# Kernel optimization log

Measured on AMD Instinct MI355X. Metric: run time of the kernel, lower is better.

The kernel has to match this reference:

```python
import jax, jax.numpy as jnp
import numpy as np

EPS = 1e-5
N_HEADS = 8


def _ln(x, g, b):
    m = jnp.mean(x, -1, keepdims=True)
    v = jnp.mean((x - m) ** 2, -1, keepdims=True)
    return (x - m) * jax.lax.rsqrt(v + EPS) * g + b


def setup_inputs() -> dict:
    key = jax.random.key(0)
    ks = jax.random.split(key, 24)
    B, T, H = 64, 512, 256
    HH, H2 = H // 2, 2 * H
    w = lambda k, shape, fan_in: jax.random.normal(k, shape, jnp.float32) / np.sqrt(fan_in)
    return {
        "state": jax.random.normal(ks[0], (B, T, H), jnp.float32),
        "action": jax.random.normal(ks[1], (B, T, 2), jnp.float32),
        "ae_w1": w(ks[2], (2, HH), 2), "ae_b1": jnp.zeros((HH,), jnp.float32),
        "ae_w2": w(ks[3], (HH, H), HH), "ae_b2": jnp.zeros((H,), jnp.float32),
        "ln1_g": jnp.ones((H,), jnp.float32), "ln1_b": jnp.zeros((H,), jnp.float32),
        "ln2_g": jnp.ones((H,), jnp.float32), "ln2_b": jnp.zeros((H,), jnp.float32),
        "wq": w(ks[4], (H, H), H), "bq": jnp.zeros((H,), jnp.float32),
        "wk": w(ks[5], (H, H), H), "bk": jnp.zeros((H,), jnp.float32),
        "wv": w(ks[6], (H, H), H), "bv": jnp.zeros((H,), jnp.float32),
        "wo": w(ks[7], (H, H), H), "bo": jnp.zeros((H,), jnp.float32),
        "gru_wih": w(ks[8], (H, 3 * H2), H), "gru_bih": jnp.zeros((3 * H2,), jnp.float32),
        "gru_whh": w(ks[9], (H2, 3 * H2), H2), "gru_bhh": jnp.zeros((3 * H2,), jnp.float32),
        "mlp_w": w(ks[10], (H2, H), H2), "mlp_b": jnp.zeros((H,), jnp.float32),
    }


def reference(state, action, ae_w1, ae_b1, ae_w2, ae_b2, ln1_g, ln1_b, ln2_g, ln2_b,
              wq, bq, wk, bk, wv, bv, wo, bo,
              gru_wih, gru_bih, gru_whh, gru_bhh, mlp_w, mlp_b):
    B, T, H = state.shape
    dH = H // N_HEADS
    # action encoder (vectorized over all timesteps at once)
    ae = jax.nn.relu(action @ ae_w1 + ae_b1) @ ae_w2 + ae_b2  # [B,T,H]
    q_in = _ln(state, ln1_g, ln1_b)
    kv_in = _ln(ae, ln2_g, ln2_b)
    qh = (q_in @ wq + bq).reshape(B, T, N_HEADS, dH)
    kh = (kv_in @ wk + bk).reshape(B, T, N_HEADS, dH)
    vh = (kv_in @ wv + bv).reshape(B, T, N_HEADS, dH)
    # single query / single key per (b,t): softmax over the length-1 key axis == 1
    scores = jnp.sum(qh * kh, -1, keepdims=True) / jnp.sqrt(jnp.asarray(dH, state.dtype))
    attn = jax.nn.softmax(scores, axis=-1)  # [B,T,nH,1] of ones
    attended = (attn * vh).reshape(B, T, H) @ wo + bo
    x = state + attended  # [B,T,H]
    # GRU: original uses batch_first=False on a [B,T,H] tensor, so the
    # recurrence runs over dim 0 (B) with T as the effective batch.
    H2 = gru_whh.shape[0]

    def step(h, x_t):  # h,[T,2H]; x_t [T,H]
        gi = x_t @ gru_wih + gru_bih
        gh = h @ gru_whh + gru_bhh
        i_r, i_z, i_n = jnp.split(gi, 3, -1)
        h_r, h_z, h_n = jnp.split(gh, 3, -1)
        r = jax.nn.sigmoid(i_r + h_r)
        z = jax.nn.sigmoid(i_z + h_z)
        n = jnp.tanh(i_n + r * h_n)
        h_new = (1.0 - z) * n + z * h
        return h_new, h_new

    h0 = jnp.zeros((T, H2), x.dtype)
    _, out = jax.lax.scan(step, h0, x)  # [B,T,2H]
    states = out @ mlp_w + mlp_b  # dropout is identity in eval mode
    return states, states[:, -1]
```

## Files before the change

kernel.cpp:

```cpp
#include <hip/hip_runtime.h>
#include <hip/hip_bf16.h>

typedef unsigned short u16;
typedef unsigned long long u64;
typedef __attribute__((ext_vector_type(8))) short bf16x8;
typedef __attribute__((ext_vector_type(4))) float f32x4;

static __device__ __forceinline__ u16 f2bf(float f) {
    union { float f; unsigned u; } cv; cv.f = f;
    unsigned u = cv.u;
    unsigned r = u + 0x7FFF + ((u >> 16) & 1);
    return (u16)(r >> 16);
}
static __device__ __forceinline__ float bf2f(u16 b) {
    union { unsigned u; float f; } cv; cv.u = ((unsigned)b) << 16;
    return cv.f;
}
static __device__ __forceinline__ float sigmoidf_(float x) {
    return 1.0f / (1.0f + __expf(-x));
}

__global__ __launch_bounds__(256) void transpose_tile_bf(
    const float* __restrict__ src, u16* __restrict__ dst, int K, int N)
{
    __shared__ u16 t[64][66];
    int k0 = blockIdx.x * 64, n0 = blockIdx.y * 64;
    int tid = threadIdx.x;
    int r = tid >> 4, c4 = (tid & 15) * 4;
#pragma unroll
    for (int p = 0; p < 4; ++p) {
        int row = r + p * 16;
        float4 v = *(const float4*)&src[(size_t)(k0 + row) * N + n0 + c4];
        t[c4 + 0][row] = f2bf(v.x);
        t[c4 + 1][row] = f2bf(v.y);
        t[c4 + 2][row] = f2bf(v.z);
        t[c4 + 3][row] = f2bf(v.w);
    }
    __syncthreads();
    int rr = tid >> 3, cc = (tid & 7) * 8;
#pragma unroll
    for (int p = 0; p < 2; ++p) {
        int row = rr + p * 32;
        u16 pack[8];
#pragma unroll
        for (int j = 0; j < 8; ++j) pack[j] = t[row][cc + j];
        *(uint4*)&dst[(size_t)(n0 + row) * K + k0 + cc] = *(uint4*)pack;
    }
}

__global__ __launch_bounds__(256) void convert_bf(
    const float* __restrict__ src, u16* __restrict__ dst)
{
    int i = (blockIdx.x * 256 + threadIdx.x) * 4;
    float4 v = *(const float4*)&src[i];
    u16 pack[4] = { f2bf(v.x), f2bf(v.y), f2bf(v.z), f2bf(v.w) };
    *(u64*)&dst[i] = *(u64*)pack;
}

__global__ __launch_bounds__(256) void bias_fuse(
    const float* __restrict__ bv, const float* __restrict__ wo,
    const float* __restrict__ bo, float* __restrict__ bfv)
{
    int j = threadIdx.x;
    float t = bo[j];
    for (int k = 0; k < 256; ++k) t = fmaf(bv[k], wo[k * 256 + j], t);
    bfv[j] = t;
}

__global__ __launch_bounds__(256) void ae_ln_mfma(
    const float* __restrict__ action,
    const float* __restrict__ w1, const float* __restrict__ b1,
    const u16* __restrict__ w2T, const float* __restrict__ b2,
    const float* __restrict__ g, const float* __restrict__ be,
    u16* __restrict__ kvbf)
{
    __shared__ u16 lB[256][136];
    __shared__ u16 lA[64][136];
    int tid = threadIdx.x;
    long base = (long)blockIdx.x * 64;

    for (int idx = tid; idx < 256 * 16; idx += 256) {
        int r = idx >> 4, ch = (idx & 15) * 8;
        *(uint4*)&lB[r][ch] = *(const uint4*)&w2T[r * 128 + ch];
    }
    for (int idx = tid; idx < 8192; idx += 256) {
        int r = idx >> 7, k = idx & 127;
        float a0 = action[(base + r) * 2], a1 = action[(base + r) * 2 + 1];
        float v = fmaf(a1, w1[128 + k], fmaf(a0, w1[k], b1[k]));
        lA[r][k] = f2bf(v > 0.f ? v : 0.f);
    }
    __syncthreads();

    int wv = tid >> 6, l = tid & 63;
    int fr = l & 15, fq = l >> 4;
    f32x4 acc[4][4] = {};
#pragma unroll
    for (int ks = 0; ks < 4; ++ks) {
        bf16x8 a[4], b[4];
#pragma unroll
        for (int mi = 0; mi < 4; ++mi) a[mi] = *(bf16x8*)&lA[mi * 16 + fr][ks * 32 + fq * 8];
#pragma unroll
        for (int ni = 0; ni < 4; ++ni) b[ni] = *(bf16x8*)&lB[wv * 64 + ni * 16 + fr][ks * 32 + fq * 8];
#pragma unroll
        for (int mi = 0; mi < 4; ++mi)
#pragma unroll
            for (int ni = 0; ni < 4; ++ni)
                acc[mi][ni] = __builtin_amdgcn_mfma_f32_16x16x32_bf16(a[mi], b[ni], acc[mi][ni], 0, 0, 0);
    }
    __syncthreads();

    float* e = (float*)&lB[0][0];
#pragma unroll
    for (int mi = 0; mi < 4; ++mi)
#pragma unroll
        for (int ni = 0; ni < 4; ++ni) {
            int col = wv * 64 + ni * 16 + fr;
            float bb = b2[col];
#pragma unroll
            for (int reg = 0; reg < 4; ++reg)
                e[(mi * 16 + fq * 4 + reg) * 261 + col] = acc[mi][ni][reg] + bb;
        }
    __syncthreads();

    int t = tid >> 2, sub = tid & 3;
    float s = 0.f, ss = 0.f;
#pragma unroll
    for (int i = 0; i < 64; ++i) {
        float v = e[t * 261 + sub + i * 4];
        s += v; ss += v * v;
    }
    s += __shfl_xor(s, 1); ss += __shfl_xor(ss, 1);
    s += __shfl_xor(s, 2); ss += __shfl_xor(ss, 2);
    float m = s * (1.f / 256.f);
    float var = ss * (1.f / 256.f) - m * m;
    float rs = rsqrtf(var + 1e-5f);
#pragma unroll
    for (int i8 = 0; i8 < 8; ++i8) {
        u16 pack[8];
#pragma unroll
        for (int j = 0; j < 8; ++j) {
            int col = sub * 64 + i8 * 8 + j;
            float v = (e[t * 261 + col] - m) * rs * g[col] + be[col];
            pack[j] = f2bf(v);
        }
        *(uint4*)&kvbf[(base + t) * 256 + sub * 64 + i8 * 8] = *(uint4*)pack;
    }
}

template <int MODE>
__global__ __launch_bounds__(256) void gemm128(
    const u16* __restrict__ A, const u16* __restrict__ BT,
    const float* __restrict__ bias, const float* __restrict__ resid,
    u16* __restrict__ outBf, float* __restrict__ outF,
    int N, int K)
{
    __shared__ u16 lA[128][72];
    __shared__ u16 lB[128][72];
    int tid = threadIdx.x;
    int bm = blockIdx.x * 128, bn = blockIdx.y * 128;

    f32x4 acc[4][4] = {};
    int w = tid >> 6, l = tid & 63;
    int wr = (w >> 1) * 64, wc = (w & 1) * 64;
    int fr = l & 15, fk = (l >> 4) * 8;

    for (int k0 = 0; k0 < K; k0 += 64) {
#pragma unroll
        for (int i = 0; i < 4; ++i) {
            int idx = tid + i * 256;
            int r = idx >> 3, c8 = (idx & 7) * 8;
            *(uint4*)&lA[r][c8] = *(const uint4*)&A[(long)(bm + r) * K + k0 + c8];
            *(uint4*)&lB[r][c8] = *(const uint4*)&BT[(long)(bn + r) * K + k0 + c8];
        }
        __syncthreads();
#pragma unroll
        for (int half = 0; half < 2; ++half) {
            int fo = half * 32 + fk;
            bf16x8 a[4], b[4];
#pragma unroll
            for (int mi = 0; mi < 4; ++mi) a[mi] = *(bf16x8*)&lA[wr + mi * 16 + fr][fo];
#pragma unroll
            for (int ni = 0; ni < 4; ++ni) b[ni] = *(bf16x8*)&lB[wc + ni * 16 + fr][fo];
#pragma unroll
            for (int mi = 0; mi < 4; ++mi)
#pragma unroll
                for (int ni = 0; ni < 4; ++ni)
                    acc[mi][ni] = __builtin_amdgcn_mfma_f32_16x16x32_bf16(a[mi], b[ni], acc[mi][ni], 0, 0, 0);
        }
        __syncthreads();
    }

#pragma unroll
    for (int mi = 0; mi < 4; ++mi)
#pragma unroll
        for (int ni = 0; ni < 4; ++ni) {
            int c = bn + wc + ni * 16 + fr;
            float bz = bias[c];
#pragma unroll
            for (int reg = 0; reg < 4; ++reg) {
                int r = bm + wr + mi * 16 + (l >> 4) * 4 + reg;
                float v = acc[mi][ni][reg] + bz;
                if constexpr (MODE == 0) {
                    v += resid[(long)r * N + c];
                    outBf[(long)r * N + c] = f2bf(v);
                } else if constexpr (MODE == 1) {
                    outBf[(long)r * N + c] = f2bf(v);
                } else {
                    outF[(long)r * N + c] = v;
                    if ((r & 511) == 511) outF[8388608 + (long)(r >> 9) * N + c] = v;
                }
            }
        }
}

__global__ __launch_bounds__(768, 1) void gru_persistent6(
    const u16* __restrict__ whhT, const float* __restrict__ bhh,
    const u16* __restrict__ gi_bf, const u16* __restrict__ h0_bf,
    u16* __restrict__ out_bf, unsigned* __restrict__ flags)
{
    __shared__ u64 lh64[2048];
    __shared__ __align__(16) float ghs[3][16][68];
    u16* lh = (u16*)lh64;

    int tid = threadIdx.x;
    int bid = blockIdx.x;
    int tg = bid >> 3, cb = bid & 7;
    int tbase = tg * 16, cbase = cb * 64;

    int w = tid >> 6, l = tid & 63;
    int fr = l & 15, fo = l >> 4;
    int cpos = w & 3, gate = w >> 2;

    bf16x8 a[16];
    {
        const u16* wp = whhT + ((size_t)(gate << 9) + cbase + cpos * 16 + fr) * 512 + fo * 8;
#pragma unroll
        for (int kk = 0; kk < 16; ++kk)
            a[kk] = *(const bf16x8*)(wp + kk * 32);
    }

    int et = tid >> 5, ec = (tid & 31) * 2;
    bool ep = tid < 512;
    float hreg0 = 0.f, hreg1 = 0.f;
    float bh_r0 = 0, bh_r1 = 0, bh_z0 = 0, bh_z1 = 0, bh_n0 = 0, bh_n1 = 0;
    if (ep) {
        bh_r0 = bhh[cbase + ec];        bh_r1 = bhh[cbase + ec + 1];
        bh_z0 = bhh[512 + cbase + ec];  bh_z1 = bhh[512 + cbase + ec + 1];
        bh_n0 = bhh[1024 + cbase + ec]; bh_n1 = bhh[1024 + cbase + ec + 1];
    }

    const unsigned* gp = (const unsigned*)gi_bf;
    unsigned g_r = 0, g_z = 0, g_n = 0;
    if (ep) {
        size_t grow = (size_t)(tbase + et) * 1536;
        g_r = gp[(grow + cbase + ec) >> 1];
        g_z = gp[(grow + 512 + cbase + ec) >> 1];
        g_n = gp[(grow + 1024 + cbase + ec) >> 1];
    }

    for (int step = 0; step < 64; ++step) {
        const u64* hb64 = (const u64*)(step ? out_bf + (size_t)(step - 1) * 262144
                                           : h0_bf);
#pragma unroll
        for (int i = 0; i < 3; ++i) {
            int idx = tid + i * 768;
            if (idx < 2048) {
                int r = idx >> 7, kw = idx & 127;
                u64 v = __hip_atomic_load(hb64 + (size_t)(tbase + r) * 128 + kw,
                                          __ATOMIC_RELAXED, __HIP_MEMORY_SCOPE_AGENT);
                lh64[r * 128 + (kw ^ ((r & 7) << 1))] = v;
            }
        }
        __syncthreads();

        f32x4 acc = {0.f, 0.f, 0.f, 0.f};
#pragma unroll
        for (int kk = 0; kk < 16; ++kk) {
            int kb = kk * 32 + fo * 8;
            bf16x8 b = *(bf16x8*)&lh[fr * 512 + (kb ^ ((fr & 7) << 3))];
            acc = __builtin_amdgcn_mfma_f32_16x16x32_bf16(a[kk], b, acc, 0, 0, 0);
        }
        *(f32x4*)&ghs[gate][fr][cpos * 16 + fo * 4] = acc;
        __syncthreads();

        if (ep) {
            float ghr0 = ghs[0][et][ec], ghr1 = ghs[0][et][ec + 1];
            float ghz0 = ghs[1][et][ec], ghz1 = ghs[1][et][ec + 1];
            float ghn0 = ghs[2][et][ec], ghn1 = ghs[2][et][ec + 1];
            float r0 = sigmoidf_(bf2f((u16)(g_r & 0xffff)) + ghr0 + bh_r0);
            float r1 = sigmoidf_(bf2f((u16)(g_r >> 16)) + ghr1 + bh_r1);
            float z0 = sigmoidf_(bf2f((u16)(g_z & 0xffff)) + ghz0 + bh_z0);
            float z1 = sigmoidf_(bf2f((u16)(g_z >> 16)) + ghz1 + bh_z1);
            float n0 = tanhf(bf2f((u16)(g_n & 0xffff)) + r0 * (ghn0 + bh_n0));
            float n1 = tanhf(bf2f((u16)(g_n >> 16)) + r1 * (ghn1 + bh_n1));
            hreg0 = (1.f - z0) * n0 + z0 * hreg0;
            hreg1 = (1.f - z1) * n1 + z1 * hreg1;
            unsigned packv = (unsigned)f2bf(hreg0) | ((unsigned)f2bf(hreg1) << 16);
            __hip_atomic_store(
                (unsigned*)out_bf + ((((size_t)step * 512 + tbase + et) * 512 + cbase + ec) >> 1),
                packv, __ATOMIC_RELAXED, __HIP_MEMORY_SCOPE_AGENT);
        }
        __syncthreads();

        if (step < 63) {
            if (tid == 0)
                __hip_atomic_store(&flags[(tg * 8 + cb) * 32], (unsigned)(step + 1),
                                   __ATOMIC_RELAXED, __HIP_MEMORY_SCOPE_AGENT);
            if (ep) {
                size_t grow = ((size_t)(step + 1) * 512 + tbase + et) * 1536;
                g_r = gp[(grow + cbase + ec) >> 1];
                g_z = gp[(grow + 512 + cbase + ec) >> 1];
                g_n = gp[(grow + 1024 + cbase + ec) >> 1];
            }
            if (tid < 8) {
                unsigned tgt = (unsigned)(step + 1);
                while (__hip_atomic_load(&flags[(tg * 8 + tid) * 32],
                                         __ATOMIC_RELAXED, __HIP_MEMORY_SCOPE_AGENT) < tgt)
                    __builtin_amdgcn_s_sleep(1);
            }
            __syncthreads();
        }
    }
}

extern "C" void kernel_launch(void* const* d_in, const int* in_sizes, int n_in,
                              void* d_out, int out_size, void* d_ws, size_t ws_size,
                              hipStream_t stream)
{
    const float* state   = (const float*)d_in[0];
    const float* action  = (const float*)d_in[1];
    const float* ae_w1   = (const float*)d_in[2];
    const float* ae_b1   = (const float*)d_in[3];
    const float* ae_w2   = (const float*)d_in[4];
    const float* ae_b2   = (const float*)d_in[5];
    const float* ln2_g   = (const float*)d_in[8];
    const float* ln2_b   = (const float*)d_in[9];
    const float* wv      = (const float*)d_in[14];
    const float* bv      = (const float*)d_in[15];
    const float* wo      = (const float*)d_in[16];
    const float* bo      = (const float*)d_in[17];
    const float* gru_wih = (const float*)d_in[18];
    const float* gru_bih = (const float*)d_in[19];
    const float* gru_whh = (const float*)d_in[20];
    const float* gru_bhh = (const float*)d_in[21];
    const float* mlp_w   = (const float*)d_in[22];
    const float* mlp_b   = (const float*)d_in[23];

    char* ws = (char*)d_ws;
    size_t off = 0;
    auto carve = [&](size_t bytes) -> char* {
        char* p = ws + off; off = (off + bytes + 255) & ~(size_t)255; return p;
    };
    u16*   kv_bf  = (u16*)carve(32768ull * 256 * 2);
    u16*   x_bf   = (u16*)carve(32768ull * 256 * 2);
    u16*   gi_bf  = (u16*)carve(32768ull * 1536 * 2);
    u16*   out_bf = (u16*)carve(32768ull * 512 * 2);
    u16*   WfT    = (u16*)carve(256 * 256 * 2);
    float* bfv    = (float*)carve(256 * 4);
    u16*   wihT   = (u16*)carve(1536 * 256 * 2);
    u16*   whhT   = (u16*)carve(1536 * 512 * 2);
    u16*   mlpT   = (u16*)carve(256 * 512 * 2);
    u16*   w2T    = (u16*)carve(256 * 128 * 2);
    u16*   woT    = (u16*)carve(256 * 256 * 2);
    u16*   wv_bf  = (u16*)carve(256 * 256 * 2);
    float* zerob  = (float*)carve(256 * 4);
    u16*   h0_bf  = (u16*)carve(512 * 512 * 2);
    unsigned* flags = (unsigned*)carve(32 * 8 * 32 * 4);

    hipMemsetAsync(h0_bf, 0, 512 * 512 * 2, stream);
    hipMemsetAsync(flags, 0, 32 * 8 * 32 * 4, stream);
    hipMemsetAsync(zerob, 0, 256 * 4, stream);

    convert_bf<<<64, 256, 0, stream>>>(wv, wv_bf);
    transpose_tile_bf<<<dim3(4, 4), 256, 0, stream>>>(wo, woT, 256, 256);
    transpose_tile_bf<<<dim3(4, 24), 256, 0, stream>>>(gru_wih, wihT, 256, 1536);
    transpose_tile_bf<<<dim3(8, 24), 256, 0, stream>>>(gru_whh, whhT, 512, 1536);
    transpose_tile_bf<<<dim3(8, 4), 256, 0, stream>>>(mlp_w, mlpT, 512, 256);
    transpose_tile_bf<<<dim3(2, 4), 256, 0, stream>>>(ae_w2, w2T, 128, 256);
    bias_fuse<<<1, 256, 0, stream>>>(bv, wo, bo, bfv);
    gemm128<1><<<dim3(2, 2), 256, 0, stream>>>(woT, wv_bf, zerob, nullptr, WfT, nullptr, 256, 256);

    ae_ln_mfma<<<512, 256, 0, stream>>>(action, ae_w1, ae_b1, w2T, ae_b2,
                                        ln2_g, ln2_b, kv_bf);

    gemm128<0><<<dim3(256, 2), 256, 0, stream>>>(kv_bf, WfT, bfv, state, x_bf, nullptr, 256, 256);
    gemm128<1><<<dim3(256, 12), 256, 0, stream>>>(x_bf, wihT, gru_bih, nullptr, gi_bf, nullptr, 1536, 256);

    {
        void* args[] = { (void*)&whhT, (void*)&gru_bhh, (void*)&gi_bf,
                         (void*)&h0_bf, (void*)&out_bf, (void*)&flags };
        hipError_t cerr = hipLaunchCooperativeKernel((const void*)gru_persistent6,
                                                     dim3(256), dim3(768), args, 0, stream);
        if (cerr != hipSuccess) {
            gru_persistent6<<<dim3(256), dim3(768), 0, stream>>>(
                whhT, gru_bhh, gi_bf, h0_bf, out_bf, flags);
        }
    }

    gemm128<2><<<dim3(256, 2), 256, 0, stream>>>(out_bf, mlpT, mlp_b, nullptr, nullptr,
                                                 (float*)d_out, 256, 512);
}
```

Baseline: 395.3 us.

## Fuse GRU input projection into persistent recurrence kernel

```diff
diff --git a/kernel.cpp b/kernel.cpp
--- a/kernel.cpp
+++ b/kernel.cpp
@@ -18,6 +18,11 @@
 }
 static __device__ __forceinline__ float sigmoidf_(float x) {
     return 1.0f / (1.0f + __expf(-x));
+}
+static __device__ __forceinline__ float tanhf_(float x) {
+    float e = __expf(-2.f * fabsf(x));
+    float t = (1.f - e) / (1.f + e);
+    return copysignf(t, x);
 }
 
 __global__ __launch_bounds__(256) void transpose_tile_bf(
@@ -213,14 +218,17 @@
         }
 }
 
-__global__ __launch_bounds__(768, 1) void gru_persistent6(
-    const u16* __restrict__ whhT, const float* __restrict__ bhh,
-    const u16* __restrict__ gi_bf, const u16* __restrict__ h0_bf,
+__global__ __launch_bounds__(768, 1) void gru_persistent8(
+    const u16* __restrict__ whhT, const u16* __restrict__ wihT,
+    const float* __restrict__ bhh, const float* __restrict__ bih,
+    const u16* __restrict__ x_bf, const u16* __restrict__ h0_bf,
     u16* __restrict__ out_bf, unsigned* __restrict__ flags)
 {
     __shared__ u64 lh64[2048];
-    __shared__ __align__(16) float ghs[3][16][68];
+    __shared__ u64 lx64[1024];
+    __shared__ __align__(16) float ghs[4][16][68];
     u16* lh = (u16*)lh64;
+    u16* lx = (u16*)lx64;
 
     int tid = threadIdx.x;
     int bid = blockIdx.x;
@@ -231,68 +239,82 @@
     int fr = l & 15, fo = l >> 4;
     int cpos = w & 3, gate = w >> 2;
 
-    bf16x8 a[16];
+    bf16x8 a[16], a2[8];
     {
         const u16* wp = whhT + ((size_t)(gate << 9) + cbase + cpos * 16 + fr) * 512 + fo * 8;
 #pragma unroll
         for (int kk = 0; kk < 16; ++kk)
             a[kk] = *(const bf16x8*)(wp + kk * 32);
+        const u16* wp2 = wihT + ((size_t)(gate << 9) + cbase + cpos * 16 + fr) * 256 + fo * 8;
+#pragma unroll
+        for (int kk = 0; kk < 8; ++kk)
+            a2[kk] = *(const bf16x8*)(wp2 + kk * 32);
     }
 
     int et = tid >> 5, ec = (tid & 31) * 2;
     bool ep = tid < 512;
     float hreg0 = 0.f, hreg1 = 0.f;
-    float bh_r0 = 0, bh_r1 = 0, bh_z0 = 0, bh_z1 = 0, bh_n0 = 0, bh_n1 = 0;
+    float bs_r0 = 0, bs_r1 = 0, bs_z0 = 0, bs_z1 = 0;
+    float bi_n0 = 0, bi_n1 = 0, bh_n0 = 0, bh_n1 = 0;
     if (ep) {
-        bh_r0 = bhh[cbase + ec];        bh_r1 = bhh[cbase + ec + 1];
-        bh_z0 = bhh[512 + cbase + ec];  bh_z1 = bhh[512 + cbase + ec + 1];
-        bh_n0 = bhh[1024 + cbase + ec]; bh_n1 = bhh[1024 + cbase + ec + 1];
-    }
-
-    const unsigned* gp = (const unsigned*)gi_bf;
-    unsigned g_r = 0, g_z = 0, g_n = 0;
-    if (ep) {
-        size_t grow = (size_t)(tbase + et) * 1536;
-        g_r = gp[(grow + cbase + ec) >> 1];
-        g_z = gp[(grow + 512 + cbase + ec) >> 1];
-        g_n = gp[(grow + 1024 + cbase + ec) >> 1];
-    }
+        bs_r0 = bih[cbase + ec] + bhh[cbase + ec];
+        bs_r1 = bih[cbase + ec + 1] + bhh[cbase + ec + 1];
+        bs_z0 = bih[512 + cbase + ec] + bhh[512 + cbase + ec];
+        bs_z1 = bih[512 + cbase + ec + 1] + bhh[512 + cbase + ec + 1];
+        bi_n0 = bih[1024 + cbase + ec];  bi_n1 = bih[1024 + cbase + ec + 1];
+        bh_n0 = bhh[1024 + cbase + ec];  bh_n1 = bhh[1024 + cbase + ec + 1];
+    }
+
+    const u64* xq = (const u64*)x_bf;
 
     for (int step = 0; step < 64; ++step) {
         const u64* hb64 = (const u64*)(step ? out_bf + (size_t)(step - 1) * 262144
                                            : h0_bf);
 #pragma unroll
-        for (int i = 0; i < 3; ++i) {
+        for (int i = 0; i < 4; ++i) {
             int idx = tid + i * 768;
             if (idx < 2048) {
                 int r = idx >> 7, kw = idx & 127;
                 u64 v = __hip_atomic_load(hb64 + (size_t)(tbase + r) * 128 + kw,
                                           __ATOMIC_RELAXED, __HIP_MEMORY_SCOPE_AGENT);
                 lh64[r * 128 + (kw ^ ((r & 7) << 1))] = v;
+            } else if (idx < 3072) {
+                int xi = idx - 2048;
+                int r = xi >> 6, kw = xi & 63;
+                u64 v = xq[((size_t)step * 512 + tbase + r) * 64 + kw];
+                lx64[r * 64 + (kw ^ ((r & 7) << 1))] = v;
             }
         }
         __syncthreads();
 
-        f32x4 acc = {0.f, 0.f, 0.f, 0.f};
+        f32x4 acch = {0.f, 0.f, 0.f, 0.f}, acci = acch;
 #pragma unroll
         for (int kk = 0; kk < 16; ++kk) {
             int kb = kk * 32 + fo * 8;
             bf16x8 b = *(bf16x8*)&lh[fr * 512 + (kb ^ ((fr & 7) << 3))];
-            acc = __builtin_amdgcn_mfma_f32_16x16x32_bf16(a[kk], b, acc, 0, 0, 0);
-        }
-        *(f32x4*)&ghs[gate][fr][cpos * 16 + fo * 4] = acc;
+            acch = __builtin_amdgcn_mfma_f32_16x16x32_bf16(a[kk], b, acch, 0, 0, 0);
+        }
+#pragma unroll
+        for (int kk = 0; kk < 8; ++kk) {
+            int kb = kk * 32 + fo * 8;
+            bf16x8 bx = *(bf16x8*)&lx[fr * 256 + (kb ^ ((fr & 7) << 3))];
+            acci = __builtin_amdgcn_mfma_f32_16x16x32_bf16(a2[kk], bx, acci, 0, 0, 0);
+        }
+        if (gate < 2) {
+            *(f32x4*)&ghs[gate][fr][cpos * 16 + fo * 4] = acch + acci;
+        } else {
+            *(f32x4*)&ghs[2][fr][cpos * 16 + fo * 4] = acci;
+            *(f32x4*)&ghs[3][fr][cpos * 16 + fo * 4] = acch;
+        }
         __syncthreads();
 
         if (ep) {
-            float ghr0 = ghs[0][et][ec], ghr1 = ghs[0][et][ec + 1];
-            float ghz0 = ghs[1][et][ec], ghz1 = ghs[1][et][ec + 1];
-            float ghn0 = ghs[2][et][ec], ghn1 = ghs[2][et][ec + 1];
-            float r0 = sigmoidf_(bf2f((u16)(g_r & 0xffff)) + ghr0 + bh_r0);
-            float r1 = sigmoidf_(bf2f((u16)(g_r >> 16)) + ghr1 + bh_r1);
-            float z0 = sigmoidf_(bf2f((u16)(g_z & 0xffff)) + ghz0 + bh_z0);
-            float z1 = sigmoidf_(bf2f((u16)(g_z >> 16)) + ghz1 + bh_z1);
-            float n0 = tanhf(bf2f((u16)(g_n & 0xffff)) + r0 * (ghn0 + bh_n0));
-            float n1 = tanhf(bf2f((u16)(g_n >> 16)) + r1 * (ghn1 + bh_n1));
+            float r0 = sigmoidf_(ghs[0][et][ec] + bs_r0);
+            float r1 = sigmoidf_(ghs[0][et][ec + 1] + bs_r1);
+            float z0 = sigmoidf_(ghs[1][et][ec] + bs_z0);
+            float z1 = sigmoidf_(ghs[1][et][ec + 1] + bs_z1);
+            float n0 = tanhf_(ghs[2][et][ec] + bi_n0 + r0 * (ghs[3][et][ec] + bh_n0));
+            float n1 = tanhf_(ghs[2][et][ec + 1] + bi_n1 + r1 * (ghs[3][et][ec + 1] + bh_n1));
             hreg0 = (1.f - z0) * n0 + z0 * hreg0;
             hreg1 = (1.f - z1) * n1 + z1 * hreg1;
             unsigned packv = (unsigned)f2bf(hreg0) | ((unsigned)f2bf(hreg1) << 16);
@@ -306,12 +328,6 @@
             if (tid == 0)
                 __hip_atomic_store(&flags[(tg * 8 + cb) * 32], (unsigned)(step + 1),
                                    __ATOMIC_RELAXED, __HIP_MEMORY_SCOPE_AGENT);
-            if (ep) {
-                size_t grow = ((size_t)(step + 1) * 512 + tbase + et) * 1536;
-                g_r = gp[(grow + cbase + ec) >> 1];
-                g_z = gp[(grow + 512 + cbase + ec) >> 1];
-                g_n = gp[(grow + 1024 + cbase + ec) >> 1];
-            }
             if (tid < 8) {
                 unsigned tgt = (unsigned)(step + 1);
                 while (__hip_atomic_load(&flags[(tg * 8 + tid) * 32],
@@ -353,7 +369,6 @@
     };
     u16*   kv_bf  = (u16*)carve(32768ull * 256 * 2);
     u16*   x_bf   = (u16*)carve(32768ull * 256 * 2);
-    u16*   gi_bf  = (u16*)carve(32768ull * 1536 * 2);
     u16*   out_bf = (u16*)carve(32768ull * 512 * 2);
     u16*   WfT    = (u16*)carve(256 * 256 * 2);
     float* bfv    = (float*)carve(256 * 4);
@@ -384,16 +399,15 @@
                                         ln2_g, ln2_b, kv_bf);
 
     gemm128<0><<<dim3(256, 2), 256, 0, stream>>>(kv_bf, WfT, bfv, state, x_bf, nullptr, 256, 256);
-    gemm128<1><<<dim3(256, 12), 256, 0, stream>>>(x_bf, wihT, gru_bih, nullptr, gi_bf, nullptr, 1536, 256);
 
     {
-        void* args[] = { (void*)&whhT, (void*)&gru_bhh, (void*)&gi_bf,
-                         (void*)&h0_bf, (void*)&out_bf, (void*)&flags };
-        hipError_t cerr = hipLaunchCooperativeKernel((const void*)gru_persistent6,
+        void* args[] = { (void*)&whhT, (void*)&wihT, (void*)&gru_bhh, (void*)&gru_bih,
+                         (void*)&x_bf, (void*)&h0_bf, (void*)&out_bf, (void*)&flags };
+        hipError_t cerr = hipLaunchCooperativeKernel((const void*)gru_persistent8,
                                                      dim3(256), dim3(768), args, 0, stream);
         if (cerr != hipSuccess) {
-            gru_persistent6<<<dim3(256), dim3(768), 0, stream>>>(
-                whhT, gru_bhh, gi_bf, h0_bf, out_bf, flags);
+            gru_persistent8<<<dim3(256), dim3(768), 0, stream>>>(
+                whhT, wihT, gru_bhh, gru_bih, x_bf, h0_bf, out_bf, flags);
         }
     }
 
```

After: 404.1 us. 2.2% more time.
